# Optimization experiments

Measured on AMD Instinct MI355X. Metric: run time of the kernel, lower is better.

## Reference

```python
import jax, jax.numpy as jnp
import numpy as np

B, T, S, H, NH, F = 16, 512, 512, 1024, 16, 4096
HD = H // NH


def _mha(x, bias, mem, wq, bq, wk, bk, wv, bv, wo, bo):
    # THUMT MultiHeadAttention: q scaled by head_dim**-0.5, additive bias on logits
    b, t, h = x.shape
    q = (x @ wq + bq) * (HD ** -0.5)
    k = mem @ wk + bk
    v = mem @ wv + bv
    split = lambda z: z.reshape(z.shape[0], z.shape[1], NH, HD).transpose(0, 2, 1, 3)
    logits = jnp.einsum('bhqd,bhkd->bhqk', split(q), split(k)) + bias
    w = jax.nn.softmax(logits, axis=-1)
    o = jnp.einsum('bhqk,bhkd->bhqd', w, split(v))
    o = o.transpose(0, 2, 1, 3).reshape(b, t, h)
    return o @ wo + bo


def _lstm(inp, w, b):
    # inp: [B, T, 2H]; gates affine over concat([x_t, h], -1): [3H] -> [4H]
    bsz = inp.shape[0]
    def step(carry, xt):
        c, hdd = carry
        g = jnp.concatenate([xt, hdd], axis=-1) @ w + b
        i, j, f, o = jnp.split(g, 4, axis=-1)
        new_c = jax.nn.sigmoid(f) * c + jax.nn.sigmoid(i) * jnp.tanh(j)
        new_h = jax.nn.sigmoid(o) * jnp.tanh(new_c)
        return (new_c, new_h), new_h
    init = (jnp.zeros((bsz, H), inp.dtype), jnp.zeros((bsz, H), inp.dtype))
    _, hs = jax.lax.scan(step, init, inp.transpose(1, 0, 2))  # [T,B,H]
    return hs.transpose(1, 0, 2)


def setup_inputs() -> dict:
    key = jax.random.key(0)
    ks = jax.random.split(key, 16)
    d = {}
    d['x'] = jax.random.normal(ks[0], (B, T, H), jnp.float32)
    d['memory'] = jax.random.normal(ks[1], (B, S, H), jnp.float32)
    d['src_bias'] = jnp.zeros((B, 1, 1, S), jnp.float32)
    causal = jnp.triu(jnp.full((T, T), -1e9, jnp.float32), k=1)
    d['tgt_bias'] = causal[None, None]
    sc = 0.02
    names = ['src_wq', 'src_wk', 'src_wv', 'src_wo', 'tgt_wq', 'tgt_wk', 'tgt_wv', 'tgt_wo']
    for i, n in enumerate(names):
        d[n] = jax.random.normal(ks[2 + i], (H, H), jnp.float32) * sc
        d[n.replace('w', 'b')] = jnp.zeros((H,), jnp.float32)
    d['lstm_w'] = jax.random.normal(ks[10], (3 * H, 4 * H), jnp.float32) * sc
    d['lstm_b'] = jnp.zeros((4 * H,), jnp.float32)
    d['ffn_w1'] = jax.random.normal(ks[11], (H, F), jnp.float32) * sc
    d['ffn_b1'] = jnp.zeros((F,), jnp.float32)
    d['ffn_w2'] = jax.random.normal(ks[12], (F, H), jnp.float32) * sc
    d['ffn_b2'] = jnp.zeros((H,), jnp.float32)
    return d


def reference(x, memory, src_bias, tgt_bias,
              src_wq, src_bq, src_wk, src_bk, src_wv, src_bv, src_wo, src_bo,
              tgt_wq, tgt_bq, tgt_wk, tgt_bk, tgt_wv, tgt_bv, tgt_wo, tgt_bo,
              lstm_w, lstm_b, ffn_w1, ffn_b1, ffn_w2, ffn_b2):
    c_src = _mha(x, src_bias, memory, src_wq, src_bq, src_wk, src_bk, src_wv, src_bv, src_wo, src_bo)
    c_tgt = _mha(x, tgt_bias, x, tgt_wq, tgt_bq, tgt_wk, tgt_bk, tgt_wv, tgt_bv, tgt_wo, tgt_bo)
    c = c_src + c_tgt  # comb_mode='sum'
    hiddens = _lstm(jnp.concatenate([x, c], axis=-1), lstm_w, lstm_b)
    hiddens = jax.nn.relu(hiddens @ ffn_w1 + ffn_b1) @ ffn_w2 + ffn_b2  # FeedForward
    return hiddens  # dropout is identity in eval
```

## Files before the change

### kernel.cpp

```cpp
#include <hip/hip_runtime.h>
#include <hip/hip_bf16.h>
#include <stdint.h>


typedef unsigned short u16;
typedef unsigned int u32;
typedef unsigned long long u64;
typedef __bf16 bf16x8 __attribute__((ext_vector_type(8)));
typedef float f32x4 __attribute__((ext_vector_type(4)));
typedef int int32x4 __attribute__((ext_vector_type(4)));
typedef unsigned long long u64x2 __attribute__((ext_vector_type(2)));

#define DEV static __device__ __forceinline__

DEV u16 f2bf(float x) {
  u32 u = __builtin_bit_cast(u32, x);
  u += 0x7FFF + ((u >> 16) & 1);
  return (u16)(u >> 16);
}

DEV bf16x8 ldfrag(const void* p) {
  int32x4 v = *(const int32x4*)p;
  return __builtin_bit_cast(bf16x8, v);
}

DEV bf16x8 mkfrag(u64 lo, u64 hi) {
  u64x2 v;
  v.x = lo;
  v.y = hi;
  return __builtin_bit_cast(bf16x8, v);
}

DEV f32x4 mfma_bf16(bf16x8 a, bf16x8 b, f32x4 c) {
  return __builtin_amdgcn_mfma_f32_16x16x32_bf16(a, b, c, 0, 0, 0);
}

DEV u64 aload(const u64* p) {
  return __hip_atomic_load(p, __ATOMIC_RELAXED, __HIP_MEMORY_SCOPE_AGENT);
}

DEV void load_lds16(const u16* g, u16* l) {
  __builtin_amdgcn_global_load_lds(
      (__attribute__((address_space(1))) void*)(uintptr_t)g,
      (__attribute__((address_space(3))) void*)(uintptr_t)l, 16, 0, 0);
}


__global__ __launch_bounds__(256) void cvt_bf16_kernel(u16* __restrict__ out,
                                                       const float* __restrict__ in,
                                                       int n4) {
  int i = blockIdx.x * 256 + threadIdx.x;
  if (i >= n4) return;
  float4 v = ((const float4*)in)[i];
  ushort4 s;
  s.x = f2bf(v.x); s.y = f2bf(v.y); s.z = f2bf(v.z); s.w = f2bf(v.w);
  ((ushort4*)out)[i] = s;
}

__global__ __launch_bounds__(256) void cvt_x_kernel(u16* __restrict__ out,
                                                    const float* __restrict__ in) {
  int i = blockIdx.x * 256 + threadIdx.x;
  int r = i >> 8, cg4 = i & 255;
  float4 v = ((const float4*)in)[i];
  ushort4 s;
  s.x = f2bf(v.x); s.y = f2bf(v.y); s.z = f2bf(v.z); s.w = f2bf(v.w);
  *(ushort4*)(out + (size_t)r * 2048 + cg4 * 4) = s;
}

__global__ __launch_bounds__(256) void convt_kernel(u16* __restrict__ out,
                                                    const float* __restrict__ in,
                                                    int K, int N, int koff, float scale) {
  __shared__ float tile[32][33];
  const int tid = threadIdx.x;
  const int n0 = blockIdx.x * 32, k0 = blockIdx.y * 32;
  const int c = tid & 31, r = tid >> 5;
#pragma unroll
  for (int i = 0; i < 4; ++i)
    tile[r + i * 8][c] = in[(size_t)(k0 + r + i * 8 + koff) * N + n0 + c];
  __syncthreads();
#pragma unroll
  for (int i = 0; i < 4; ++i)
    out[(size_t)(n0 + r + i * 8) * K + k0 + c] = f2bf(tile[c][r + i * 8] * scale);
}

__global__ __launch_bounds__(256) void convt_perm_kernel(u16* __restrict__ out,
                                                         const float* __restrict__ in,
                                                         int K, int koff) {
  __shared__ float tile[32][33];
  const int tid = threadIdx.x;
  const int u0 = blockIdx.x * 32, k0 = blockIdx.y * 32, g = blockIdx.z;
  const int c = tid & 31, r = tid >> 5;
#pragma unroll
  for (int i = 0; i < 4; ++i)
    tile[r + i * 8][c] = in[(size_t)(k0 + r + i * 8 + koff) * 4096 + g * 1024 + u0 + c];
  __syncthreads();
#pragma unroll
  for (int i = 0; i < 4; ++i)
    out[(size_t)((u0 + r + i * 8) * 4 + g) * K + k0 + c] = f2bf(tile[c][r + i * 8]);
}

__global__ __launch_bounds__(256) void pack_bias_kernel(float* __restrict__ out,
                                                        const float* __restrict__ in) {
  int p = blockIdx.x * 256 + threadIdx.x;
  out[p] = in[(p & 3) * 1024 + (p >> 2)];
}

__global__ __launch_bounds__(256) void pack_bias3_kernel(
    float* __restrict__ out, const float* __restrict__ b0,
    const float* __restrict__ b1, const float* __restrict__ b2, float s0) {
  int p = blockIdx.x * 256 + threadIdx.x;
  float v = (p < 1024) ? b0[p] * s0 : (p < 2048 ? b1[p - 1024] : b2[p - 2048]);
  out[p] = v;
}

template <int OUTBF, int ACCUM, int RELU, int PERM>
__global__ __launch_bounds__(256) void gemm_bt_kernel(
    const u16* __restrict__ A, int lda, const u16* __restrict__ Bt,
    const float* __restrict__ bias, float bscale,
    void* __restrict__ outp, int ostride,
    const float* __restrict__ cacc, int cstride, int K) {
  __shared__ u16 As[128 * 32];
  __shared__ u16 Bs[128 * 32];
  const int tid = threadIdx.x;
  const int wave = tid >> 6, lane = tid & 63;
  const int lr = lane & 15, lg = lane >> 4;
  const int nwg = gridDim.x * gridDim.y;
  const int wgid = blockIdx.y * gridDim.x + blockIdx.x;
  const int swz = (wgid & 7) * (nwg >> 3) + (wgid >> 3);
  const int m0 = (swz / gridDim.x) * 128, n0 = (swz % gridDim.x) * 128;
  const int wr = (wave >> 1) * 64, wc = (wave & 1) * 64;

  f32x4 acc[4][4] = {};

  const int sr = lane >> 2, sce = (lane & 3) * 8;
  const u16* gA = A + (size_t)(m0 + wave * 16 + sr) * lda + sce;
  const u16* gB = Bt + (size_t)(n0 + wave * 16 + sr) * K + sce;
  u16* lA = As + wave * 16 * 32;
  u16* lB = Bs + wave * 16 * 32;

  for (int k0 = 0; k0 < K; k0 += 32) {
    __syncthreads();
    load_lds16(gA + k0, lA);
    load_lds16(gA + k0 + (size_t)64 * lda, lA + 64 * 32);
    load_lds16(gB + k0, lB);
    load_lds16(gB + k0 + (size_t)64 * K, lB + 64 * 32);
    __syncthreads();
    bf16x8 af[4], bfr[4];
    const u16* pa = As + (wr + lr) * 32 + lg * 8;
    const u16* pb = Bs + (wc + lr) * 32 + lg * 8;
#pragma unroll
    for (int i = 0; i < 4; ++i) af[i] = ldfrag(pa + i * 16 * 32);
#pragma unroll
    for (int j = 0; j < 4; ++j) bfr[j] = ldfrag(pb + j * 16 * 32);
#pragma unroll
    for (int i = 0; i < 4; ++i)
#pragma unroll
      for (int j = 0; j < 4; ++j)
        acc[i][j] = mfma_bf16(af[i], bfr[j], acc[i][j]);
  }

  const int col0 = n0 + wc + lr;
  const int row0 = m0 + wr + lg * 4;
#pragma unroll
  for (int i = 0; i < 4; ++i) {
#pragma unroll
    for (int j = 0; j < 4; ++j) {
      const int c = col0 + j * 16;
      const float bv = bias ? bias[c] * bscale : 0.f;
#pragma unroll
      for (int ii = 0; ii < 4; ++ii) {
        const int r = row0 + i * 16 + ii;
        float v = acc[i][j][ii] + bv;
        if (ACCUM) v += cacc[(size_t)r * cstride + c];
        if (RELU) v = fmaxf(v, 0.f);
        const int rp = (PERM == 2) ? ((r & 15) * 512 + (r >> 4)) : r;
        if (OUTBF) ((u16*)outp)[(size_t)rp * ostride + c] = f2bf(v);
        else       ((float*)outp)[(size_t)rp * ostride + c] = v;
      }
    }
  }
}

template <int CAUSAL>
__global__ __launch_bounds__(256) void flash_kernel(
    const u16* __restrict__ Q, const u16* __restrict__ Kb, const u16* __restrict__ Vb,
    const float* __restrict__ sbias, u16* __restrict__ O, int qs, int ks) {
  __shared__ u16 Kl[64 * 72];
  __shared__ u16 Vt[64 * 72];
  __shared__ u16 Pl[64 * 72];
  const int tid = threadIdx.x, wave = tid >> 6, lane = tid & 63;
  const int lr = lane & 15, lg = lane >> 4;
  const int q0 = blockIdx.x * 64, hh = blockIdx.y, b = blockIdx.z;

  bf16x8 qf[2];
  {
    const u16* qp = Q + (size_t)(b * 512 + q0 + wave * 16 + lr) * qs + hh * 64 + lg * 8;
    qf[0] = ldfrag(qp);
    qf[1] = ldfrag(qp + 32);
  }
  f32x4 oacc[4] = {};
  float mrun[4], lsum[4];
#pragma unroll
  for (int ii = 0; ii < 4; ++ii) { mrun[ii] = -3e38f; lsum[ii] = 0.f; }

  const int ntiles = CAUSAL ? (q0 / 64 + 1) : 8;
  for (int ti = 0; ti < ntiles; ++ti) {
    const int s0 = ti * 64;
    {
      const int r = tid >> 2, ch = (tid & 3) * 16;
      const u16* kp = Kb + (size_t)(b * 512 + s0 + r) * ks + hh * 64 + ch;
      const u16* vp = Vb + (size_t)(b * 512 + s0 + r) * ks + hh * 64 + ch;
      int32x4 k0v = *(const int32x4*)kp;
      int32x4 k1v = *(const int32x4*)(kp + 8);
      int32x4 v0v = *(const int32x4*)vp;
      int32x4 v1v = *(const int32x4*)(vp + 8);
      *(int32x4*)&Kl[r * 72 + ch] = k0v;
      *(int32x4*)&Kl[r * 72 + ch + 8] = k1v;
      const u16* v0p = (const u16*)&v0v;
      const u16* v1p = (const u16*)&v1v;
#pragma unroll
      for (int j = 0; j < 8; ++j) {
        Vt[(ch + j) * 72 + r] = v0p[j];
        Vt[(ch + 8 + j) * 72 + r] = v1p[j];
      }
    }
    __syncthreads();
    f32x4 sf[4] = {};
#pragma unroll
    for (int j = 0; j < 4; ++j)
#pragma unroll
      for (int ks2 = 0; ks2 < 2; ++ks2) {
        bf16x8 kf = ldfrag(&Kl[(j * 16 + lr) * 72 + ks2 * 32 + lg * 8]);
        sf[j] = mfma_bf16(qf[ks2], kf, sf[j]);
      }
    if (!CAUSAL) {
#pragma unroll
      for (int j = 0; j < 4; ++j) {
        const float bv = sbias[b * 512 + s0 + j * 16 + lr];
#pragma unroll
        for (int ii = 0; ii < 4; ++ii) sf[j][ii] += bv;
      }
    } else {
#pragma unroll
      for (int j = 0; j < 4; ++j) {
        const int s = s0 + j * 16 + lr;
#pragma unroll
        for (int ii = 0; ii < 4; ++ii) {
          const int q = q0 + wave * 16 + lg * 4 + ii;
          if (s > q) sf[j][ii] -= 1e9f;
        }
      }
    }
    float sc[4], rs[4];
#pragma unroll
    for (int ii = 0; ii < 4; ++ii) {
      float m = fmaxf(fmaxf(sf[0][ii], sf[1][ii]), fmaxf(sf[2][ii], sf[3][ii]));
#pragma unroll
      for (int off = 1; off < 16; off <<= 1) m = fmaxf(m, __shfl_xor(m, off));
      const float mn = fmaxf(mrun[ii], m);
      sc[ii] = __expf(mrun[ii] - mn);
      mrun[ii] = mn;
      rs[ii] = 0.f;
    }
#pragma unroll
    for (int j = 0; j < 4; ++j)
#pragma unroll
      for (int ii = 0; ii < 4; ++ii) {
        const float p = __expf(sf[j][ii] - mrun[ii]);
        rs[ii] += p;
        Pl[(wave * 16 + lg * 4 + ii) * 72 + j * 16 + lr] = f2bf(p);
      }
#pragma unroll
    for (int ii = 0; ii < 4; ++ii) {
      float r = rs[ii];
#pragma unroll
      for (int off = 1; off < 16; off <<= 1) r += __shfl_xor(r, off);
      lsum[ii] = lsum[ii] * sc[ii] + r;
    }
#pragma unroll
    for (int df = 0; df < 4; ++df)
#pragma unroll
      for (int ii = 0; ii < 4; ++ii) oacc[df][ii] *= sc[ii];
    __syncthreads();
    bf16x8 pf[2];
    pf[0] = ldfrag(&Pl[(wave * 16 + lr) * 72 + lg * 8]);
    pf[1] = ldfrag(&Pl[(wave * 16 + lr) * 72 + 32 + lg * 8]);
#pragma unroll
    for (int df = 0; df < 4; ++df)
#pragma unroll
      for (int ks2 = 0; ks2 < 2; ++ks2) {
        bf16x8 vf = ldfrag(&Vt[(df * 16 + lr) * 72 + ks2 * 32 + lg * 8]);
        oacc[df] = mfma_bf16(pf[ks2], vf, oacc[df]);
      }
    __syncthreads();
  }
#pragma unroll
  for (int df = 0; df < 4; ++df)
#pragma unroll
    for (int ii = 0; ii < 4; ++ii) {
      const float v = oacc[df][ii] / lsum[ii];
      O[(size_t)(b * 512 + q0 + wave * 16 + lg * 4 + ii) * 1024 + hh * 64 + df * 16 + lr] =
          f2bf(v);
    }
}

#define SCAN_NW 32
__global__ __launch_bounds__(256, 1) void lstm_scan_kernel(
    const u16* __restrict__ Whp, const float* __restrict__ gx,
    u16* __restrict__ hbuf) {
  const int tid = threadIdx.x, wave = tid >> 6, lane = tid & 63;
  const int lr = lane & 15, lg = lane >> 4;
  const int g = blockIdx.x;
  __shared__ float part[2][4][16][132];
  const int gb = tid >> 4;
  const int up = tid & 15;
  float cs0 = 0.f, cs1 = 0.f;
  const u64 SENT = 0xFFFFFFFFFFFFFFFFull;

  const u16* wbase = Whp + (size_t)(g * 128 + lr) * 1024 + wave * 256 + lg * 8;
  const float* gxp = gx + (size_t)gb * 512 * 4096 + g * 128 + up * 8;
  const size_t goff = (size_t)lr * 1024 + wave * 256 + lg * 8;

  for (int t = 0; t < 512; ++t) {
    const float4 gxv0 = *(const float4*)(gxp + (size_t)t * 4096);
    const float4 gxv1 = *(const float4*)(gxp + (size_t)t * 4096 + 4);
    const u16* hp = hbuf + (size_t)t * 16384 + goff;
    u64 hw[16];
#pragma unroll
    for (int kc = 0; kc < 8; ++kc) {
      hw[kc * 2] = aload((const u64*)(hp + kc * 32));
      hw[kc * 2 + 1] = aload((const u64*)(hp + kc * 32 + 4));
    }
    {
      int guard = 0;
      for (;;) {
        bool ok = true;
#pragma unroll
        for (int i = 0; i < 16; ++i) ok &= (hw[i] != SENT);
        if (__all((int)ok)) break;
        __builtin_amdgcn_s_sleep(4);
        if (++guard > (1 << 20)) break;
#pragma unroll
        for (int kc = 0; kc < 8; ++kc) {
          if (hw[kc * 2] == SENT)
            hw[kc * 2] = aload((const u64*)(hp + kc * 32));
          if (hw[kc * 2 + 1] == SENT)
            hw[kc * 2 + 1] = aload((const u64*)(hp + kc * 32 + 4));
        }
      }
    }
    f32x4 acc[8] = {};
#pragma unroll
    for (int kc = 0; kc < 8; ++kc) {
      const bf16x8 hf = mkfrag(hw[kc * 2], hw[kc * 2 + 1]);
#pragma unroll
      for (int j = 0; j < 8; ++j)
        acc[j] = mfma_bf16(hf, ldfrag(wbase + j * 16 * 1024 + kc * 32), acc[j]);
    }
    const int p = t & 1;
#pragma unroll
    for (int j = 0; j < 8; ++j)
#pragma unroll
      for (int ii = 0; ii < 4; ++ii)
        part[p][wave][lg * 4 + ii][j * 16 + lr] = acc[j][ii];
    __syncthreads();
    float s[8];
#pragma unroll
    for (int k = 0; k < 8; ++k)
      s[k] = part[p][0][gb][up * 8 + k] + part[p][1][gb][up * 8 + k] +
             part[p][2][gb][up * 8 + k] + part[p][3][gb][up * 8 + k];
    float hA, hB;
    {
      const float si = s[0] + gxv0.x, sj = s[1] + gxv0.y;
      const float sf_ = s[2] + gxv0.z, so = s[3] + gxv0.w;
      const float ig = 1.f / (1.f + __expf(-si));
      const float jg = 1.f - 2.f / (__expf(2.f * sj) + 1.f);
      const float fg = 1.f / (1.f + __expf(-sf_));
      const float og = 1.f / (1.f + __expf(-so));
      cs0 = fg * cs0 + ig * jg;
      hA = og * (1.f - 2.f / (__expf(2.f * cs0) + 1.f));
    }
    {
      const float si = s[4] + gxv1.x, sj = s[5] + gxv1.y;
      const float sf_ = s[6] + gxv1.z, so = s[7] + gxv1.w;
      const float ig = 1.f / (1.f + __expf(-si));
      const float jg = 1.f - 2.f / (__expf(2.f * sj) + 1.f);
      const float fg = 1.f / (1.f + __expf(-sf_));
      const float og = 1.f / (1.f + __expf(-so));
      cs1 = fg * cs1 + ig * jg;
      hB = og * (1.f - 2.f / (__expf(2.f * cs1) + 1.f));
    }
    const u32 myw = (u32)f2bf(hA) | ((u32)f2bf(hB) << 16);
    const u32 otherw = (u32)__shfl_down((int)myw, 1);
    if (!(up & 1)) {
      u64 w64 = (u64)myw | ((u64)otherw << 32);
      u64* dst = (u64*)(hbuf + (size_t)(t + 1) * 16384 + (size_t)gb * 1024 +
                        g * 32 + up * 2);
      __hip_atomic_store(dst, w64, __ATOMIC_RELAXED, __HIP_MEMORY_SCOPE_AGENT);
    }
  }
}


extern "C" void kernel_launch(void* const* d_in, const int* in_sizes, int n_in,
                              void* d_out, int out_size, void* d_ws, size_t ws_size,
                              hipStream_t stream) {
  const float* x        = (const float*)d_in[0];
  const float* mem      = (const float*)d_in[1];
  const float* src_bias = (const float*)d_in[2];
  const float* w_src_q = (const float*)d_in[4];  const float* b_src_q = (const float*)d_in[5];
  const float* w_src_k = (const float*)d_in[6];  const float* b_src_k = (const float*)d_in[7];
  const float* w_src_v = (const float*)d_in[8];  const float* b_src_v = (const float*)d_in[9];
  const float* w_src_o = (const float*)d_in[10]; const float* b_src_o = (const float*)d_in[11];
  const float* w_tgt_q = (const float*)d_in[12]; const float* b_tgt_q = (const float*)d_in[13];
  const float* w_tgt_k = (const float*)d_in[14]; const float* b_tgt_k = (const float*)d_in[15];
  const float* w_tgt_v = (const float*)d_in[16]; const float* b_tgt_v = (const float*)d_in[17];
  const float* w_tgt_o = (const float*)d_in[18]; const float* b_tgt_o = (const float*)d_in[19];
  const float* lstm_w  = (const float*)d_in[20]; const float* lstm_b  = (const float*)d_in[21];
  const float* w1 = (const float*)d_in[22]; const float* b1f = (const float*)d_in[23];
  const float* w2 = (const float*)d_in[24]; const float* b2f = (const float*)d_in[25];

  char* ws = (char*)d_ws;
  const size_t MiB = 1024ull * 1024ull;
  u16*   xcb  = (u16*)(ws + 0);
  u16*   wlp  = (u16*)(ws + 32 * MiB);
  u16*   whp  = (u16*)(ws + 48 * MiB);
  u16*   w1t  = (u16*)(ws + 56 * MiB);
  u16*   w2t  = (u16*)(ws + 64 * MiB);
  float* pb   = (float*)(ws + 72 * MiB);
  float* pb3  = pb + 4096;
  float* pb2  = pb3 + 3072;
  u16*   hbuf = (u16*)(ws + 73 * MiB);
  u16*   memb = (u16*)(ws + 90 * MiB);
  u16*   wt[8];
  for (int i = 0; i < 8; ++i) wt[i] = (u16*)(ws + 106 * MiB + (size_t)i * 2 * MiB);
  u16*   qsrc = (u16*)(ws + 122 * MiB);
  u16*   kvs  = (u16*)(ws + 138 * MiB);
  u16*   qkv  = (u16*)(ws + 122 * MiB);
  u16*   ao_s = (u16*)(ws + 170 * MiB);
  u16*   ao_t = (u16*)(ws + 186 * MiB);
  float* c32  = (float*)(ws + 202 * MiB);
  float* gx   = (float*)(ws + 90 * MiB);
  u16*   ffn1 = (u16*)(ws + 90 * MiB);

  hipMemsetAsync(hbuf + 16384, 0xFF, (size_t)512 * 16384 * 2, stream);
  hipMemsetAsync(hbuf, 0, 32768, stream);

  cvt_x_kernel<<<8192, 256, 0, stream>>>(xcb, x);
  cvt_bf16_kernel<<<8192, 256, 0, stream>>>(memb, mem, 2097152);
  const dim3 g1k(32, 32);
  convt_kernel<<<g1k, 256, 0, stream>>>(wt[0], w_src_q, 1024, 1024, 0, 0.125f);
  convt_kernel<<<g1k, 256, 0, stream>>>(wt[1], w_src_k, 1024, 1024, 0, 1.f);
  convt_kernel<<<g1k, 256, 0, stream>>>(wt[2], w_src_v, 1024, 1024, 0, 1.f);
  convt_kernel<<<g1k, 256, 0, stream>>>(wt[3], w_src_o, 1024, 1024, 0, 1.f);
  convt_kernel<<<g1k, 256, 0, stream>>>(wt[4], w_tgt_q, 1024, 1024, 0, 0.125f);
  convt_kernel<<<g1k, 256, 0, stream>>>(wt[5], w_tgt_k, 1024, 1024, 0, 1.f);
  convt_kernel<<<g1k, 256, 0, stream>>>(wt[6], w_tgt_v, 1024, 1024, 0, 1.f);
  convt_kernel<<<g1k, 256, 0, stream>>>(wt[7], w_tgt_o, 1024, 1024, 0, 1.f);
  convt_perm_kernel<<<dim3(32, 64, 4), 256, 0, stream>>>(wlp, lstm_w, 2048, 0);
  convt_perm_kernel<<<dim3(32, 32, 4), 256, 0, stream>>>(whp, lstm_w, 1024, 2048);
  convt_kernel<<<dim3(128, 32), 256, 0, stream>>>(w1t, w1, 1024, 4096, 0, 1.f);
  convt_kernel<<<dim3(32, 128), 256, 0, stream>>>(w2t, w2, 4096, 1024, 0, 1.f);
  pack_bias_kernel<<<16, 256, 0, stream>>>(pb, lstm_b);
  pack_bias3_kernel<<<12, 256, 0, stream>>>(pb3, b_tgt_q, b_tgt_k, b_tgt_v, 0.125f);
  pack_bias3_kernel<<<8, 256, 0, stream>>>(pb2, b_src_k, b_src_v, b_src_v, 1.f);

  gemm_bt_kernel<1, 0, 0, 0><<<dim3(8, 64), 256, 0, stream>>>(xcb, 2048, wt[0], b_src_q, 0.125f, qsrc, 1024, nullptr, 0, 1024);
  gemm_bt_kernel<1, 0, 0, 0><<<dim3(16, 64), 256, 0, stream>>>(memb, 1024, wt[1], pb2, 1.f, kvs, 2048, nullptr, 0, 1024);
  flash_kernel<0><<<dim3(8, 16, 16), 256, 0, stream>>>(qsrc, kvs, kvs + 1024, src_bias, ao_s, 1024, 2048);
  gemm_bt_kernel<1, 0, 0, 0><<<dim3(24, 64), 256, 0, stream>>>(xcb, 2048, wt[4], pb3, 1.f, qkv, 3072, nullptr, 0, 1024);
  flash_kernel<1><<<dim3(8, 16, 16), 256, 0, stream>>>(qkv, qkv + 1024, qkv + 2048, nullptr, ao_t, 3072, 3072);
  gemm_bt_kernel<0, 0, 0, 0><<<dim3(8, 64), 256, 0, stream>>>(ao_s, 1024, wt[3], b_src_o, 1.f, c32, 1024, nullptr, 0, 1024);
  gemm_bt_kernel<1, 1, 0, 0><<<dim3(8, 64), 256, 0, stream>>>(ao_t, 1024, wt[7], b_tgt_o, 1.f, xcb + 1024, 2048, c32, 1024, 1024);
  gemm_bt_kernel<0, 0, 0, 0><<<dim3(32, 64), 256, 0, stream>>>(xcb, 2048, wlp, pb, 1.f, gx, 4096, nullptr, 0, 2048);
  lstm_scan_kernel<<<dim3(SCAN_NW), 256, 0, stream>>>(whp, gx, hbuf);
  gemm_bt_kernel<1, 0, 1, 0><<<dim3(32, 64), 256, 0, stream>>>(hbuf + 16384, 1024, w1t, b1f, 1.f, ffn1, 4096, nullptr, 0, 1024);
  gemm_bt_kernel<0, 0, 0, 2><<<dim3(8, 64), 256, 0, stream>>>(ffn1, 4096, w2t, b2f, 1.f, (float*)d_out, 1024, nullptr, 0, 4096);
}
```

Baseline: 2.956 ms.

## Fuse Q/QKV projections and output projections, store LSTM input gates in bf16

Merges the src-Q and tgt-QKV projections into one wide GEMM and concatenates both attention outputs so that a single K=2048 GEMM with a summed bias produces the combined context. This removes the fp32 intermediate c32 and the accumulate pass. The precomputed LSTM input-gate activations are now stored as bf16 instead of fp32, which halves the per-step gx traffic in the serial scan but loses precision. The scan's spin-wait sleep is also shortened.

```diff
diff --git a/kernel.cpp b/kernel.cpp
--- a/kernel.cpp
+++ b/kernel.cpp
@@ -10,6 +10,7 @@
 typedef float f32x4 __attribute__((ext_vector_type(4)));
 typedef int int32x4 __attribute__((ext_vector_type(4)));
 typedef unsigned long long u64x2 __attribute__((ext_vector_type(2)));
+typedef unsigned short u16x8 __attribute__((ext_vector_type(8)));
 
 #define DEV static __device__ __forceinline__
 
@@ -105,20 +106,36 @@
   out[p] = in[(p & 3) * 1024 + (p >> 2)];
 }
 
-__global__ __launch_bounds__(256) void pack_bias3_kernel(
-    float* __restrict__ out, const float* __restrict__ b0,
-    const float* __restrict__ b1, const float* __restrict__ b2, float s0) {
+__global__ __launch_bounds__(256) void pack_bias2_kernel(
+    float* __restrict__ out, const float* __restrict__ a,
+    const float* __restrict__ b, float s) {
   int p = blockIdx.x * 256 + threadIdx.x;
-  float v = (p < 1024) ? b0[p] * s0 : (p < 2048 ? b1[p - 1024] : b2[p - 2048]);
+  out[p] = (p < 1024) ? a[p] * s : b[p - 1024];
+}
+
+__global__ __launch_bounds__(256) void pack_bias4_kernel(
+    float* __restrict__ out, const float* __restrict__ a,
+    const float* __restrict__ b, const float* __restrict__ c,
+    const float* __restrict__ d, float s) {
+  int p = blockIdx.x * 256 + threadIdx.x;
+  float v = (p < 1024)   ? a[p] * s
+            : (p < 2048) ? b[p - 1024] * s
+            : (p < 3072) ? c[p - 2048]
+                         : d[p - 3072];
   out[p] = v;
 }
 
-template <int OUTBF, int ACCUM, int RELU, int PERM>
+__global__ __launch_bounds__(256) void bias_sum_kernel(float* __restrict__ out,
+                                                       const float* __restrict__ a,
+                                                       const float* __restrict__ b) {
+  int p = blockIdx.x * 256 + threadIdx.x;
+  out[p] = a[p] + b[p];
+}
+
+template <int OUTBF, int RELU, int PERM>
 __global__ __launch_bounds__(256) void gemm_bt_kernel(
     const u16* __restrict__ A, int lda, const u16* __restrict__ Bt,
-    const float* __restrict__ bias, float bscale,
-    void* __restrict__ outp, int ostride,
-    const float* __restrict__ cacc, int cstride, int K) {
+    const float* __restrict__ bias, void* __restrict__ outp, int ostride, int K) {
   __shared__ u16 As[128 * 32];
   __shared__ u16 Bs[128 * 32];
   const int tid = threadIdx.x;
@@ -166,12 +183,11 @@
 #pragma unroll
     for (int j = 0; j < 4; ++j) {
       const int c = col0 + j * 16;
-      const float bv = bias ? bias[c] * bscale : 0.f;
+      const float bv = bias ? bias[c] : 0.f;
 #pragma unroll
       for (int ii = 0; ii < 4; ++ii) {
         const int r = row0 + i * 16 + ii;
         float v = acc[i][j][ii] + bv;
-        if (ACCUM) v += cacc[(size_t)r * cstride + c];
         if (RELU) v = fmaxf(v, 0.f);
         const int rp = (PERM == 2) ? ((r & 15) * 512 + (r >> 4)) : r;
         if (OUTBF) ((u16*)outp)[(size_t)rp * ostride + c] = f2bf(v);
@@ -184,7 +200,7 @@
 template <int CAUSAL>
 __global__ __launch_bounds__(256) void flash_kernel(
     const u16* __restrict__ Q, const u16* __restrict__ Kb, const u16* __restrict__ Vb,
-    const float* __restrict__ sbias, u16* __restrict__ O, int qs, int ks) {
+    const float* __restrict__ sbias, u16* __restrict__ O, int qs, int ks, int ost) {
   __shared__ u16 Kl[64 * 72];
   __shared__ u16 Vt[64 * 72];
   __shared__ u16 Pl[64 * 72];
@@ -299,14 +315,14 @@
 #pragma unroll
     for (int ii = 0; ii < 4; ++ii) {
       const float v = oacc[df][ii] / lsum[ii];
-      O[(size_t)(b * 512 + q0 + wave * 16 + lg * 4 + ii) * 1024 + hh * 64 + df * 16 + lr] =
+      O[(size_t)(b * 512 + q0 + wave * 16 + lg * 4 + ii) * ost + hh * 64 + df * 16 + lr] =
           f2bf(v);
     }
 }
 
 #define SCAN_NW 32
 __global__ __launch_bounds__(256, 1) void lstm_scan_kernel(
-    const u16* __restrict__ Whp, const float* __restrict__ gx,
+    const u16* __restrict__ Whp, const u16* __restrict__ gxb,
     u16* __restrict__ hbuf) {
   const int tid = threadIdx.x, wave = tid >> 6, lane = tid & 63;
   const int lr = lane & 15, lg = lane >> 4;
@@ -318,12 +334,11 @@
   const u64 SENT = 0xFFFFFFFFFFFFFFFFull;
 
   const u16* wbase = Whp + (size_t)(g * 128 + lr) * 1024 + wave * 256 + lg * 8;
-  const float* gxp = gx + (size_t)gb * 512 * 4096 + g * 128 + up * 8;
+  const u16* gxp = gxb + (size_t)gb * 512 * 4096 + g * 128 + up * 8;
   const size_t goff = (size_t)lr * 1024 + wave * 256 + lg * 8;
 
   for (int t = 0; t < 512; ++t) {
-    const float4 gxv0 = *(const float4*)(gxp + (size_t)t * 4096);
-    const float4 gxv1 = *(const float4*)(gxp + (size_t)t * 4096 + 4);
+    const bf16x8 gxv = ldfrag(gxp + (size_t)t * 4096);
     const u16* hp = hbuf + (size_t)t * 16384 + goff;
     u64 hw[16];
 #pragma unroll
@@ -338,7 +353,7 @@
 #pragma unroll
         for (int i = 0; i < 16; ++i) ok &= (hw[i] != SENT);
         if (__all((int)ok)) break;
-        __builtin_amdgcn_s_sleep(4);
+        __builtin_amdgcn_s_sleep(2);
         if (++guard > (1 << 20)) break;
 #pragma unroll
         for (int kc = 0; kc < 8; ++kc) {
@@ -369,10 +384,15 @@
     for (int k = 0; k < 8; ++k)
       s[k] = part[p][0][gb][up * 8 + k] + part[p][1][gb][up * 8 + k] +
              part[p][2][gb][up * 8 + k] + part[p][3][gb][up * 8 + k];
+    const u16x8 gq = __builtin_bit_cast(u16x8, gxv);
+    float gxf[8];
+#pragma unroll
+    for (int k = 0; k < 8; ++k)
+      gxf[k] = __builtin_bit_cast(float, (u32)((u32)gq[k] << 16));
     float hA, hB;
     {
-      const float si = s[0] + gxv0.x, sj = s[1] + gxv0.y;
-      const float sf_ = s[2] + gxv0.z, so = s[3] + gxv0.w;
+      const float si = s[0] + gxf[0], sj = s[1] + gxf[1];
+      const float sf_ = s[2] + gxf[2], so = s[3] + gxf[3];
       const float ig = 1.f / (1.f + __expf(-si));
       const float jg = 1.f - 2.f / (__expf(2.f * sj) + 1.f);
       const float fg = 1.f / (1.f + __expf(-sf_));
@@ -381,8 +401,8 @@
       hA = og * (1.f - 2.f / (__expf(2.f * cs0) + 1.f));
     }
     {
-      const float si = s[4] + gxv1.x, sj = s[5] + gxv1.y;
-      const float sf_ = s[6] + gxv1.z, so = s[7] + gxv1.w;
+      const float si = s[4] + gxf[4], sj = s[5] + gxf[5];
+      const float sf_ = s[6] + gxf[6], so = s[7] + gxf[7];
       const float ig = 1.f / (1.f + __expf(-si));
       const float jg = 1.f - 2.f / (__expf(2.f * sj) + 1.f);
       const float fg = 1.f / (1.f + __expf(-sf_));
@@ -428,20 +448,19 @@
   u16*   w1t  = (u16*)(ws + 56 * MiB);
   u16*   w2t  = (u16*)(ws + 64 * MiB);
   float* pb   = (float*)(ws + 72 * MiB);
-  float* pb3  = pb + 4096;
-  float* pb2  = pb3 + 3072;
+  float* pbq4 = pb + 4096;
+  float* pb2  = pbq4 + 4096;
+  float* pbo  = pb2 + 2048;
   u16*   hbuf = (u16*)(ws + 73 * MiB);
   u16*   memb = (u16*)(ws + 90 * MiB);
-  u16*   wt[8];
-  for (int i = 0; i < 8; ++i) wt[i] = (u16*)(ws + 106 * MiB + (size_t)i * 2 * MiB);
-  u16*   qsrc = (u16*)(ws + 122 * MiB);
-  u16*   kvs  = (u16*)(ws + 138 * MiB);
-  u16*   qkv  = (u16*)(ws + 122 * MiB);
-  u16*   ao_s = (u16*)(ws + 170 * MiB);
-  u16*   ao_t = (u16*)(ws + 186 * MiB);
-  float* c32  = (float*)(ws + 202 * MiB);
-  float* gx   = (float*)(ws + 90 * MiB);
-  u16*   ffn1 = (u16*)(ws + 90 * MiB);
+  u16*   aot2 = (u16*)(ws + 90 * MiB);
+  u16*   gxb  = (u16*)(ws + 90 * MiB);
+  u16*   qx4  = (u16*)(ws + 122 * MiB);
+  u16*   kvs  = (u16*)(ws + 186 * MiB);
+  u16*   wqt4 = (u16*)(ws + 218 * MiB);
+  u16*   wkv2 = (u16*)(ws + 226 * MiB);
+  u16*   wo2  = (u16*)(ws + 230 * MiB);
+  u16*   ffn1 = (u16*)(ws + 154 * MiB);
 
   hipMemsetAsync(hbuf + 16384, 0xFF, (size_t)512 * 16384 * 2, stream);
   hipMemsetAsync(hbuf, 0, 32768, stream);
@@ -449,31 +468,30 @@
   cvt_x_kernel<<<8192, 256, 0, stream>>>(xcb, x);
   cvt_bf16_kernel<<<8192, 256, 0, stream>>>(memb, mem, 2097152);
   const dim3 g1k(32, 32);
-  convt_kernel<<<g1k, 256, 0, stream>>>(wt[0], w_src_q, 1024, 1024, 0, 0.125f);
-  convt_kernel<<<g1k, 256, 0, stream>>>(wt[1], w_src_k, 1024, 1024, 0, 1.f);
-  convt_kernel<<<g1k, 256, 0, stream>>>(wt[2], w_src_v, 1024, 1024, 0, 1.f);
-  convt_kernel<<<g1k, 256, 0, stream>>>(wt[3], w_src_o, 1024, 1024, 0, 1.f);
-  convt_kernel<<<g1k, 256, 0, stream>>>(wt[4], w_tgt_q, 1024, 1024, 0, 0.125f);
-  convt_kernel<<<g1k, 256, 0, stream>>>(wt[5], w_tgt_k, 1024, 1024, 0, 1.f);
-  convt_kernel<<<g1k, 256, 0, stream>>>(wt[6], w_tgt_v, 1024, 1024, 0, 1.f);
-  convt_kernel<<<g1k, 256, 0, stream>>>(wt[7], w_tgt_o, 1024, 1024, 0, 1.f);
+  convt_kernel<<<g1k, 256, 0, stream>>>(wqt4,                w_src_q, 1024, 1024, 0, 0.125f);
+  convt_kernel<<<g1k, 256, 0, stream>>>(wqt4 + 1 * 1048576,  w_tgt_q, 1024, 1024, 0, 0.125f);
+  convt_kernel<<<g1k, 256, 0, stream>>>(wqt4 + 2 * 1048576,  w_tgt_k, 1024, 1024, 0, 1.f);
+  convt_kernel<<<g1k, 256, 0, stream>>>(wqt4 + 3 * 1048576,  w_tgt_v, 1024, 1024, 0, 1.f);
+  convt_kernel<<<g1k, 256, 0, stream>>>(wkv2,                w_src_k, 1024, 1024, 0, 1.f);
+  convt_kernel<<<g1k, 256, 0, stream>>>(wkv2 + 1048576,      w_src_v, 1024, 1024, 0, 1.f);
+  convt_kernel<<<g1k, 256, 0, stream>>>(wo2,                 w_src_o, 2048, 1024, 0, 1.f);
+  convt_kernel<<<g1k, 256, 0, stream>>>(wo2 + 1024,          w_tgt_o, 2048, 1024, 0, 1.f);
   convt_perm_kernel<<<dim3(32, 64, 4), 256, 0, stream>>>(wlp, lstm_w, 2048, 0);
   convt_perm_kernel<<<dim3(32, 32, 4), 256, 0, stream>>>(whp, lstm_w, 1024, 2048);
   convt_kernel<<<dim3(128, 32), 256, 0, stream>>>(w1t, w1, 1024, 4096, 0, 1.f);
   convt_kernel<<<dim3(32, 128), 256, 0, stream>>>(w2t, w2, 4096, 1024, 0, 1.f);
   pack_bias_kernel<<<16, 256, 0, stream>>>(pb, lstm_b);
-  pack_bias3_kernel<<<12, 256, 0, stream>>>(pb3, b_tgt_q, b_tgt_k, b_tgt_v, 0.125f);
-  pack_bias3_kernel<<<8, 256, 0, stream>>>(pb2, b_src_k, b_src_v, b_src_v, 1.f);
-
-  gemm_bt_kernel<1, 0, 0, 0><<<dim3(8, 64), 256, 0, stream>>>(xcb, 2048, wt[0], b_src_q, 0.125f, qsrc, 1024, nullptr, 0, 1024);
-  gemm_bt_kernel<1, 0, 0, 0><<<dim3(16, 64), 256, 0, stream>>>(memb, 1024, wt[1], pb2, 1.f, kvs, 2048, nullptr, 0, 1024);
-  flash_kernel<0><<<dim3(8, 16, 16), 256, 0, stream>>>(qsrc, kvs, kvs + 1024, src_bias, ao_s, 1024, 2048);
-  gemm_bt_kernel<1, 0, 0, 0><<<dim3(24, 64), 256, 0, stream>>>(xcb, 2048, wt[4], pb3, 1.f, qkv, 3072, nullptr, 0, 1024);
-  flash_kernel<1><<<dim3(8, 16, 16), 256, 0, stream>>>(qkv, qkv + 1024, qkv + 2048, nullptr, ao_t, 3072, 3072);
-  gemm_bt_kernel<0, 0, 0, 0><<<dim3(8, 64), 256, 0, stream>>>(ao_s, 1024, wt[3], b_src_o, 1.f, c32, 1024, nullptr, 0, 1024);
-  gemm_bt_kernel<1, 1, 0, 0><<<dim3(8, 64), 256, 0, stream>>>(ao_t, 1024, wt[7], b_tgt_o, 1.f, xcb + 1024, 2048, c32, 1024, 1024);
-  gemm_bt_kernel<0, 0, 0, 0><<<dim3(32, 64), 256, 0, stream>>>(xcb, 2048, wlp, pb, 1.f, gx, 4096, nullptr, 0, 2048);
-  lstm_scan_kernel<<<dim3(SCAN_NW), 256, 0, stream>>>(whp, gx, hbuf);
-  gemm_bt_kernel<1, 0, 1, 0><<<dim3(32, 64), 256, 0, stream>>>(hbuf + 16384, 1024, w1t, b1f, 1.f, ffn1, 4096, nullptr, 0, 1024);
-  gemm_bt_kernel<0, 0, 0, 2><<<dim3(8, 64), 256, 0, stream>>>(ffn1, 4096, w2t, b2f, 1.f, (float*)d_out, 1024, nullptr, 0, 4096);
-}
+  pack_bias4_kernel<<<16, 256, 0, stream>>>(pbq4, b_src_q, b_tgt_q, b_tgt_k, b_tgt_v, 0.125f);
+  pack_bias2_kernel<<<8, 256, 0, stream>>>(pb2, b_src_k, b_src_v, 1.f);
+  bias_sum_kernel<<<4, 256, 0, stream>>>(pbo, b_src_o, b_tgt_o);
+
+  gemm_bt_kernel<1, 0, 0><<<dim3(32, 64), 256, 0, stream>>>(xcb, 2048, wqt4, pbq4, qx4, 4096, 1024);
+  gemm_bt_kernel<1, 0, 0><<<dim3(16, 64), 256, 0, stream>>>(memb, 1024, wkv2, pb2, kvs, 2048, 1024);
+  flash_kernel<0><<<dim3(8, 16, 16), 256, 0, stream>>>(qx4, kvs, kvs + 1024, src_bias, aot2, 4096, 2048, 2048);
+  flash_kernel<1><<<dim3(8, 16, 16), 256, 0, stream>>>(qx4 + 1024, qx4 + 2048, qx4 + 3072, nullptr, aot2 + 1024, 4096, 4096, 2048);
+  gemm_bt_kernel<1, 0, 0><<<dim3(8, 64), 256, 0, stream>>>(aot2, 2048, wo2, pbo, xcb + 1024, 2048, 2048);
+  gemm_bt_kernel<1, 0, 0><<<dim3(32, 64), 256, 0, stream>>>(xcb, 2048, wlp, pb, gxb, 4096, 2048);
+  lstm_scan_kernel<<<dim3(SCAN_NW), 256, 0, stream>>>(whp, gxb, hbuf);
+  gemm_bt_kernel<1, 1, 0><<<dim3(32, 64), 256, 0, stream>>>(hbuf + 16384, 1024, w1t, b1f, ffn1, 4096, 1024);
+  gemm_bt_kernel<0, 0, 2><<<dim3(8, 64), 256, 0, stream>>>(ffn1, 4096, w2t, b2f, (float*)d_out, 1024, 4096);
+}
```

Result: no change. 2.950 ms (-0.2%).
